# Kernel optimization log

Hardware: AMD Instinct MI355X
Metric: run time of the kernel (lower is better)

The kernel has to match this reference:

```python
import jax, jax.numpy as jnp
import numpy as np

D_MODEL = 1024
N_HEADS = 16
HEAD_DIM = D_MODEL // N_HEADS
D_FF = 4096
B, S = 2, 2048
EPS = 1e-6
NEG = -1e9


def setup_inputs() -> dict:
    key = jax.random.key(0)
    ks = jax.random.split(key, 16)
    sd = 1.0 / np.sqrt(D_MODEL)
    sf = 1.0 / np.sqrt(D_FF)
    inp = {
        "x": jax.random.normal(ks[0], (B, S, D_MODEL), jnp.float32),
        # causal mask, broadcastable over batch and heads
        "mask": jnp.tril(jnp.ones((S, S), jnp.bool_))[None, None, :, :],
        # attention projections, torch Linear layout [out, in]
        "Wq": jax.random.normal(ks[1], (D_MODEL, D_MODEL), jnp.float32) * sd,
        "bq": jnp.zeros((D_MODEL,), jnp.float32),
        "Wk": jax.random.normal(ks[2], (D_MODEL, D_MODEL), jnp.float32) * sd,
        "bk": jnp.zeros((D_MODEL,), jnp.float32),
        "Wv": jax.random.normal(ks[3], (D_MODEL, D_MODEL), jnp.float32) * sd,
        "bv": jnp.zeros((D_MODEL,), jnp.float32),
        "Wo": jax.random.normal(ks[4], (D_MODEL, D_MODEL), jnp.float32) * sd,
        "bo": jnp.zeros((D_MODEL,), jnp.float32),
        # layer norms
        "ln1_g": jnp.ones((D_MODEL,), jnp.float32),
        "ln1_b": jnp.zeros((D_MODEL,), jnp.float32),
        "ln2_g": jnp.ones((D_MODEL,), jnp.float32),
        "ln2_b": jnp.zeros((D_MODEL,), jnp.float32),
        # FFN
        "W1": jax.random.normal(ks[5], (D_FF, D_MODEL), jnp.float32) * sd,
        "b1": jnp.zeros((D_FF,), jnp.float32),
        "W2": jax.random.normal(ks[6], (D_MODEL, D_FF), jnp.float32) * sf,
        "b2": jnp.zeros((D_MODEL,), jnp.float32),
    }
    return inp


def _layer_norm(x, g, b):
    mu = jnp.mean(x, axis=-1, keepdims=True)
    var = jnp.var(x, axis=-1, keepdims=True)
    return (x - mu) * jax.lax.rsqrt(var + EPS) * g + b


def _linear(x, W, b):
    return jnp.einsum('...i,oi->...o', x, W) + b


def _attention(x, mask, Wq, bq, Wk, bk, Wv, bv, Wo, bo):
    Bsz, Sq, _ = x.shape
    q = _linear(x, Wq, bq).reshape(Bsz, Sq, N_HEADS, HEAD_DIM)
    k = _linear(x, Wk, bk).reshape(Bsz, Sq, N_HEADS, HEAD_DIM)
    v = _linear(x, Wv, bv).reshape(Bsz, Sq, N_HEADS, HEAD_DIM)
    # [B,H,S,S]
    scores = jnp.einsum('bqhd,bkhd->bhqk', q, k) / np.sqrt(HEAD_DIM)
    scores = jnp.where(mask, scores, NEG)
    weights = jax.nn.softmax(scores, axis=-1)
    ctx = jnp.einsum('bhqk,bkhd->bqhd', weights, v).reshape(Bsz, Sq, D_MODEL)
    return _linear(ctx, Wo, bo)


def reference(x, mask, Wq, bq, Wk, bk, Wv, bv, Wo, bo,
              ln1_g, ln1_b, ln2_g, ln2_b, W1, b1, W2, b2):
    # pre-LN attention block (dropout = identity at inference)
    h = _layer_norm(x, ln1_g, ln1_b)
    x = x + _attention(h, mask, Wq, bq, Wk, bk, Wv, bv, Wo, bo)
    # pre-LN FFN block
    h = _layer_norm(x, ln2_g, ln2_b)
    h = jax.nn.gelu(_linear(h, W1, b1), approximate=False)
    x = x + _linear(h, W2, b2)
    return x
```

## Files before the change

kernel.cpp:

```cpp
#include <hip/hip_runtime.h>
#include <hip/hip_bf16.h>
#include <cstdint>
#include <cstddef>

typedef unsigned short u16;
typedef __bf16 bf16x8 __attribute__((ext_vector_type(8)));
typedef float f32x4 __attribute__((ext_vector_type(4)));

#define D_MODEL 1024
#define D_FF    4096
#define BATCH   2
#define SEQ     2048
#define NH      16
#define HD      64
#define ROWS    (BATCH*SEQ)
#define QKVS    3072

__device__ __forceinline__ u16 f2bf(float f) {
    union { float f; uint32_t u; } v; v.f = f;
    uint32_t u = v.u;
    u += 0x7FFF + ((u >> 16) & 1);
    return (u16)(u >> 16);
}

__device__ __forceinline__ float bf2f(u16 u) {
    union { uint32_t u; float f; } v; v.u = (uint32_t)u << 16;
    return v.f;
}

__device__ __forceinline__ uint32_t cvtpk_bf16(float lo, float hi) {
    uint32_t r;
    asm("v_cvt_pk_bf16_f32 %0, %1, %2" : "=v"(r) : "v"(lo), "v"(hi));
    return r;
}

__device__ __forceinline__ bf16x8 ldg8(const u16* p) {
    return *reinterpret_cast<const bf16x8*>(p);
}

__device__ __forceinline__ f32x4 mfma16(bf16x8 a, bf16x8 b, f32x4 c) {
    return __builtin_amdgcn_mfma_f32_16x16x32_bf16(a, b, c, 0, 0, 0);
}

__device__ __forceinline__ void gld_lds16(const void* g, void* l) {
    __builtin_amdgcn_global_load_lds(
        (const __attribute__((address_space(1))) void*)g,
        (__attribute__((address_space(3))) void*)l, 16, 0, 0);
}

__device__ __forceinline__ float gelu_f(float x) {
    float u = fmaf(0.044715f * x, x * x, x);
    float z = fminf(-2.3022036f * u, 126.0f);
    float e = __builtin_amdgcn_exp2f(z);
    return x / (1.0f + e);
}

struct alignas(8) U16x4 { u16 x, y, z, w; };

__global__ __launch_bounds__(256) void prep(
    const float* __restrict__ s0, const float* __restrict__ s1,
    const float* __restrict__ s2, const float* __restrict__ s3,
    const float* __restrict__ s4, const float* __restrict__ s5,
    u16* __restrict__ wout,
    const float* __restrict__ x, const float* __restrict__ g1,
    const float* __restrict__ be1, u16* __restrict__ hbuf,
    const float* __restrict__ bq, const float* __restrict__ bk,
    const float* __restrict__ bv, float* __restrict__ bqkv)
{
    const size_t MM1 = 1 << 20;
    const int bid = blockIdx.x;
    const int t = threadIdx.x;

    if (bid < 12288) {
        size_t i = (size_t)bid * 1024 + t * 4;
        const float* src; size_t off;
        if      (i <     MM1) { src = s0; off = i; }
        else if (i < 2 * MM1) { src = s1; off = i - MM1; }
        else if (i < 3 * MM1) { src = s2; off = i - 2 * MM1; }
        else if (i < 4 * MM1) { src = s3; off = i - 3 * MM1; }
        else if (i < 8 * MM1) { src = s4; off = i - 4 * MM1; }
        else                  { src = s5; off = i - 8 * MM1; }
        float4 f = *reinterpret_cast<const float4*>(src + off);
        U16x4 o{ f2bf(f.x), f2bf(f.y), f2bf(f.z), f2bf(f.w) };
        *reinterpret_cast<U16x4*>(wout + i) = o;
    } else if (bid < 12288 + ROWS) {
        int row = bid - 12288;
        const float* xr = x + (size_t)row * D_MODEL;
        float4 v = *reinterpret_cast<const float4*>(xr + t * 4);
        float s = v.x + v.y + v.z + v.w;
        float q = v.x*v.x + v.y*v.y + v.z*v.z + v.w*v.w;
        #pragma unroll
        for (int off = 1; off < 64; off <<= 1) {
            s += __shfl_xor(s, off);
            q += __shfl_xor(q, off);
        }
        __shared__ float red[8];
        if ((t & 63) == 0) { red[(t >> 6) * 2] = s; red[(t >> 6) * 2 + 1] = q; }
        __syncthreads();
        float sum = red[0] + red[2] + red[4] + red[6];
        float sq  = red[1] + red[3] + red[5] + red[7];
        float mu  = sum * (1.0f / D_MODEL);
        float var = sq * (1.0f / D_MODEL) - mu * mu;
        float rstd = rsqrtf(var + 1e-6f);
        float4 gg = *reinterpret_cast<const float4*>(g1 + t * 4);
        float4 bb = *reinterpret_cast<const float4*>(be1 + t * 4);
        U16x4 o{ f2bf((v.x - mu) * rstd * gg.x + bb.x),
                 f2bf((v.y - mu) * rstd * gg.y + bb.y),
                 f2bf((v.z - mu) * rstd * gg.z + bb.z),
                 f2bf((v.w - mu) * rstd * gg.w + bb.w) };
        *reinterpret_cast<U16x4*>(hbuf + (size_t)row * D_MODEL + t * 4) = o;
    } else {
        int j = bid - (12288 + ROWS);
        const float* src = (j == 0) ? bq : (j == 1) ? bk : bv;
        float4 f = *reinterpret_cast<const float4*>(src + t * 4);
        *reinterpret_cast<float4*>(bqkv + j * 1024 + t * 4) = f;
    }
}

__global__ __launch_bounds__(256) void ln2_bf16(
    const u16* __restrict__ x, const float* __restrict__ g,
    const float* __restrict__ b, u16* __restrict__ out)
{
    int row = blockIdx.x;
    const u16* xr = x + (size_t)row * D_MODEL;
    int t = threadIdx.x;
    U16x4 u = *reinterpret_cast<const U16x4*>(xr + t * 4);
    float vx = bf2f(u.x), vy = bf2f(u.y), vz = bf2f(u.z), vw = bf2f(u.w);
    float s = vx + vy + vz + vw;
    float q = vx*vx + vy*vy + vz*vz + vw*vw;
    #pragma unroll
    for (int off = 1; off < 64; off <<= 1) {
        s += __shfl_xor(s, off);
        q += __shfl_xor(q, off);
    }
    __shared__ float red[8];
    if ((t & 63) == 0) { red[(t >> 6) * 2] = s; red[(t >> 6) * 2 + 1] = q; }
    __syncthreads();
    float sum = red[0] + red[2] + red[4] + red[6];
    float sq  = red[1] + red[3] + red[5] + red[7];
    float mu  = sum * (1.0f / D_MODEL);
    float var = sq * (1.0f / D_MODEL) - mu * mu;
    float rstd = rsqrtf(var + 1e-6f);
    float4 gg = *reinterpret_cast<const float4*>(g + t * 4);
    float4 bb = *reinterpret_cast<const float4*>(b + t * 4);
    U16x4 o{ f2bf((vx - mu) * rstd * gg.x + bb.x),
             f2bf((vy - mu) * rstd * gg.y + bb.y),
             f2bf((vz - mu) * rstd * gg.z + bb.z),
             f2bf((vw - mu) * rstd * gg.w + bb.w) };
    *reinterpret_cast<U16x4*>(out + (size_t)row * D_MODEL + t * 4) = o;
}

#define EPI_BF16   0
#define EPI_RESF32 1
#define EPI_GELU   2
#define EPI_PART   3
#define EPI_QKV    4
#define EPI_RESB16 5

template<int EPI>
__global__ __launch_bounds__(256, 4) void gemm97(
    const u16* __restrict__ A, const u16* __restrict__ B,
    const float* __restrict__ bias, const float* __restrict__ res,
    u16* __restrict__ outb, float* __restrict__ outf,
    int M, int N, int K, int KS)
{
    __shared__ u16 As[128 * 64];
    __shared__ u16 Bs[128 * 64];
    const int t = threadIdx.x;
    const int lane = t & 63, w = t >> 6;
    const int lr = lane & 15, lg = lane >> 4;
    const int wrr = (w >> 1) * 64, wcc = (w & 1) * 64;
    const int brow = blockIdx.x * 128, bcol = blockIdx.y * 128;
    const u16* Ag = A + (size_t)brow * KS;
    const u16* Bg = B + (size_t)bcol * KS;

    f32x4 acc[4][4] = {};
    const int NT = K >> 6;

    for (int kt = 0; kt < NT; ++kt) {
        #pragma unroll
        for (int c = 0; c < 4; ++c) {
            int f = c * 256 + t;
            int row = f >> 3, slot = f & 7;
            int sg = slot ^ (row & 7);
            gld_lds16(Ag + (size_t)row * KS + kt * 64 + sg * 8, As + f * 8);
            gld_lds16(Bg + (size_t)row * KS + kt * 64 + sg * 8, Bs + f * 8);
        }
        __syncthreads();

        bf16x8 af[4][2];
        #pragma unroll
        for (int mi = 0; mi < 4; ++mi) {
            int row = wrr + mi * 16 + lr;
            const u16* bp = As + row * 64;
            int key = row & 7;
            af[mi][0] = ldg8(bp + ((0 + lg) ^ key) * 8);
            af[mi][1] = ldg8(bp + ((4 + lg) ^ key) * 8);
        }
        __builtin_amdgcn_s_setprio(1);
        #pragma unroll
        for (int ni = 0; ni < 4; ++ni) {
            int row = wcc + ni * 16 + lr;
            const u16* bp = Bs + row * 64;
            int key = row & 7;
            bf16x8 b0 = ldg8(bp + ((0 + lg) ^ key) * 8);
            bf16x8 b1 = ldg8(bp + ((4 + lg) ^ key) * 8);
            #pragma unroll
            for (int mi = 0; mi < 4; ++mi) {
                acc[mi][ni] = mfma16(af[mi][0], b0, acc[mi][ni]);
                acc[mi][ni] = mfma16(af[mi][1], b1, acc[mi][ni]);
            }
        }
        __builtin_amdgcn_s_setprio(0);
        __syncthreads();
    }

    #pragma unroll
    for (int mi = 0; mi < 4; ++mi) {
        int r0 = brow + wrr + mi * 16 + lg * 4;
        #pragma unroll
        for (int ni = 0; ni < 4; ++ni) {
            int c = bcol + wcc + ni * 16 + lr;
            float bv = bias[c];
            if constexpr (EPI == EPI_QKV) {
                if (bcol >= 2048) {
                    U16x4 pk{ f2bf(acc[mi][ni][0] + bv), f2bf(acc[mi][ni][1] + bv),
                              f2bf(acc[mi][ni][2] + bv), f2bf(acc[mi][ni][3] + bv) };
                    int d = c - 2048;
                    int bb = r0 >> 11, s = r0 & 2047;
                    u16* vt = (u16*)outf;
                    *reinterpret_cast<U16x4*>(
                        vt + ((size_t)(bb * NH + (d >> 6)) * HD + (d & 63)) * SEQ + s) = pk;
                    continue;
                }
            }
            #pragma unroll
            for (int j = 0; j < 4; ++j) {
                float v = acc[mi][ni][j] + bv;
                size_t idx = (size_t)(r0 + j) * N + c;
                if constexpr (EPI == EPI_GELU) {
                    outb[idx] = f2bf(gelu_f(v));
                } else if constexpr (EPI == EPI_RESF32) {
                    outf[idx] = v + res[idx];
                } else {
                    outb[idx] = f2bf(v);
                }
            }
        }
    }
}

template<int EPI, int RM>
__global__ __launch_bounds__(256, 2) void gemm_bt(
    const u16* __restrict__ A, const u16* __restrict__ B,
    const float* __restrict__ bias, const float* __restrict__ res,
    u16* __restrict__ outb, float* __restrict__ outf,
    int M, int N, int K, int KS)
{
    __shared__ u16 As[2][128 * 64];
    __shared__ u16 Bs[2][128 * 64];
    const int t = threadIdx.x;
    const int lane = t & 63;
    const int w = t >> 6;
    const int lr = lane & 15, lg = lane >> 4;
    const int wrr = (w >> 1) * 64, wcc = (w & 1) * 64;
    const int brow = (RM ? blockIdx.x : blockIdx.y) * 128;
    const int bcol = (RM ? blockIdx.y : blockIdx.x) * 128;
    const int kz = blockIdx.z;
    const u16* Ag = A + (size_t)brow * KS + (size_t)kz * K;
    const u16* Bg = B + (size_t)bcol * KS + (size_t)kz * K;

    f32x4 acc[4][4] = {};

    const int NT = K >> 6;

    auto stage = [&](int buf, int kt) {
        const u16* ga = Ag + kt * 64;
        const u16* gb = Bg + kt * 64;
        u16* la = As[buf];
        u16* lb = Bs[buf];
        #pragma unroll
        for (int c = 0; c < 4; ++c) {
            int f = c * 256 + t;
            int row = f >> 3, slot = f & 7;
            int sg = slot ^ (row & 7);
            gld_lds16(ga + (size_t)row * KS + sg * 8, la + f * 8);
            gld_lds16(gb + (size_t)row * KS + sg * 8, lb + f * 8);
        }
    };

    auto compute = [&](int buf) {
        const u16* la = As[buf];
        const u16* lb = Bs[buf];
        bf16x8 af[4][2];
        #pragma unroll
        for (int mi = 0; mi < 4; ++mi) {
            int row = wrr + mi * 16 + lr;
            int base = row * 64;
            af[mi][0] = *reinterpret_cast<const bf16x8*>(la + base + ((0 + lg) ^ (row & 7)) * 8);
            af[mi][1] = *reinterpret_cast<const bf16x8*>(la + base + ((4 + lg) ^ (row & 7)) * 8);
        }
        __builtin_amdgcn_s_setprio(1);
        #pragma unroll
        for (int ni = 0; ni < 4; ++ni) {
            int row = wcc + ni * 16 + lr;
            int base = row * 64;
            bf16x8 b0 = *reinterpret_cast<const bf16x8*>(lb + base + ((0 + lg) ^ (row & 7)) * 8);
            bf16x8 b1 = *reinterpret_cast<const bf16x8*>(lb + base + ((4 + lg) ^ (row & 7)) * 8);
            #pragma unroll
            for (int mi = 0; mi < 4; ++mi) {
                acc[mi][ni] = mfma16(af[mi][0], b0, acc[mi][ni]);
                acc[mi][ni] = mfma16(af[mi][1], b1, acc[mi][ni]);
            }
        }
        __builtin_amdgcn_s_setprio(0);
    };

    stage(0, 0);
    if (NT > 1) {
        stage(1, 1);
        asm volatile("s_waitcnt vmcnt(8)" ::: "memory");
    } else {
        asm volatile("s_waitcnt vmcnt(0)" ::: "memory");
    }
    __builtin_amdgcn_s_barrier();

    for (int kt = 0; kt < NT; ++kt) {
        compute(kt & 1);
        if (kt + 1 == NT) break;
        __builtin_amdgcn_s_barrier();
        if (kt + 2 < NT) {
            stage(kt & 1, kt + 2);
            asm volatile("s_waitcnt vmcnt(8)" ::: "memory");
        } else {
            asm volatile("s_waitcnt vmcnt(0)" ::: "memory");
        }
        __builtin_amdgcn_s_barrier();
    }

    #pragma unroll
    for (int mi = 0; mi < 4; ++mi) {
        int r0 = brow + wrr + mi * 16 + lg * 4;
        #pragma unroll
        for (int ni = 0; ni < 4; ++ni) {
            int c = bcol + wcc + ni * 16 + lr;
            float bv = 0.f;
            if constexpr (EPI != EPI_PART) bv = bias[c];
            #pragma unroll
            for (int j = 0; j < 4; ++j) {
                float v = acc[mi][ni][j] + bv;
                size_t idx = (size_t)(r0 + j) * N + c;
                if constexpr (EPI == EPI_GELU) {
                    outb[idx] = f2bf(gelu_f(v));
                } else if constexpr (EPI == EPI_RESF32) {
                    outf[idx] = v + res[idx];
                } else if constexpr (EPI == EPI_RESB16) {
                    outb[idx] = f2bf(v + res[idx]);
                } else if constexpr (EPI == EPI_PART) {
                    outb[idx + (size_t)kz * M * N] = f2bf(v);
                } else {
                    outb[idx] = f2bf(v);
                }
            }
        }
    }
}

__global__ void ffn2_reduce(const u16* __restrict__ p,
                            const float* __restrict__ b2,
                            const u16* __restrict__ x2,
                            float* __restrict__ out)
{
    size_t i = ((size_t)blockIdx.x * 256 + threadIdx.x) * 4;
    U16x4 a0 = *reinterpret_cast<const U16x4*>(p + i);
    U16x4 a1 = *reinterpret_cast<const U16x4*>(p + (size_t)ROWS * D_MODEL + i);
    U16x4 rr = *reinterpret_cast<const U16x4*>(x2 + i);
    float4 bb = *reinterpret_cast<const float4*>(b2 + (i & (D_MODEL - 1)));
    float4 o;
    o.x = bf2f(a0.x) + bf2f(a1.x) + bf2f(rr.x) + bb.x;
    o.y = bf2f(a0.y) + bf2f(a1.y) + bf2f(rr.y) + bb.y;
    o.z = bf2f(a0.z) + bf2f(a1.z) + bf2f(rr.z) + bb.z;
    o.w = bf2f(a0.w) + bf2f(a1.w) + bf2f(rr.w) + bb.w;
    *reinterpret_cast<float4*>(out + i) = o;
}

#define QBLK  64
#define KVBLK 64

__global__ __launch_bounds__(256, 3) void attn8(
    const u16* __restrict__ QKV, const u16* __restrict__ VT,
    u16* __restrict__ O)
{
    __shared__ u16 Ks[3][64 * 64];
    __shared__ u16 Vs[2][64 * 64];
    __shared__ u16 Pl[4][16 * 72];

    const int i  = blockIdx.x;
    const int bh = blockIdx.y;
    const int b = bh >> 4, h = bh & 15;
    const int qta = 31 - i;
    const int qtb = i;
    const int q0a = qta * QBLK, q0b = qtb * QBLK;
    const int t = threadIdx.x;
    const int lane = t & 63, w = t >> 6;
    const int lr = lane & 15, lg = lane >> 4;

    const size_t rowbase = (size_t)b * SEQ;
    const u16* Qg = QKV + rowbase * QKVS + h * HD;
    const u16* Kg = Qg + 1024;
    const u16* Vg = VT + (size_t)bh * HD * SEQ;

    const u16* qpa = Qg + (size_t)(q0a + w * 16 + lr) * QKVS;
    const u16* qpb = Qg + (size_t)(q0b + w * 16 + lr) * QKVS;
    bf16x8 qa0 = ldg8(qpa + lg * 8), qa1 = ldg8(qpa + 32 + lg * 8);
    bf16x8 qb0 = ldg8(qpb + lg * 8), qb1 = ldg8(qpb + 32 + lg * 8);

    f32x4 oa[4] = {}, ob[4] = {};
    float lsa[4] = {}, lsb[4] = {};

    const int ntiles = qta + 1;
    u16* Pw = Pl[w];
    const float SC = 0.125f * 1.44269504089f;

    auto stageK = [&](int buf, int tt) {
        const int kv0 = tt * KVBLK;
        #pragma unroll
        for (int c = 0; c < 2; ++c) {
            int f = c * 256 + t;
            int row = f >> 3, slot = f & 7;
            int sgk = slot ^ ((row >> 2) & 7);
            gld_lds16(Kg + (size_t)(kv0 + row) * QKVS + sgk * 8, Ks[buf] + f * 8);
        }
    };
    auto stageV = [&](int buf, int tt) {
        const int kv0 = tt * KVBLK;
        #pragma unroll
        for (int c = 0; c < 2; ++c) {
            int f = c * 256 + t;
            int row = f >> 3, slot = f & 7;
            int sgv = slot ^ (row & 7);
            gld_lds16(Vg + (size_t)row * SEQ + kv0 + sgv * 8, Vs[buf] + f * 8);
        }
    };

    auto qtile = [&](bf16x8 qf0, bf16x8 qf1, f32x4* o, float* ls,
                     int q0, int kv0, bool diag, const u16* kb, const u16* vb) {
        f32x4 s[4] = {};
        __builtin_amdgcn_s_setprio(1);
        #pragma unroll
        for (int ni = 0; ni < 4; ++ni) {
            int row = lr * 4 + ni;
            const u16* base = kb + row * 64;
            int key = (row >> 2) & 7;
            bf16x8 k0 = *reinterpret_cast<const bf16x8*>(base + ((0 + lg) ^ key) * 8);
            bf16x8 k1 = *reinterpret_cast<const bf16x8*>(base + ((4 + lg) ^ key) * 8);
            s[ni] = mfma16(qf0, k0, s[ni]);
            s[ni] = mfma16(qf1, k1, s[ni]);
        }
        __builtin_amdgcn_s_setprio(0);

        #pragma unroll
        for (int j = 0; j < 4; ++j) {
            int qi = q0 + w * 16 + lg * 4 + j;
            float p0 = __builtin_amdgcn_exp2f(s[0][j] * SC);
            float p1 = __builtin_amdgcn_exp2f(s[1][j] * SC);
            float p2 = __builtin_amdgcn_exp2f(s[2][j] * SC);
            float p3 = __builtin_amdgcn_exp2f(s[3][j] * SC);
            if (diag) {
                int kvb = kv0 + lr * 4;
                p0 = (kvb     <= qi) ? p0 : 0.f;
                p1 = (kvb + 1 <= qi) ? p1 : 0.f;
                p2 = (kvb + 2 <= qi) ? p2 : 0.f;
                p3 = (kvb + 3 <= qi) ? p3 : 0.f;
            }
            ls[j] += (p0 + p1) + (p2 + p3);
            uint2 pk = make_uint2(cvtpk_bf16(p0, p1), cvtpk_bf16(p2, p3));
            *reinterpret_cast<uint2*>(&Pw[(lg * 4 + j) * 72 + lr * 4]) = pk;
        }

        bf16x8 pa0 = *reinterpret_cast<const bf16x8*>(Pw + lr * 72 + lg * 8);
        bf16x8 pa1 = *reinterpret_cast<const bf16x8*>(Pw + lr * 72 + 32 + lg * 8);
        __builtin_amdgcn_s_setprio(1);
        #pragma unroll
        for (int ni = 0; ni < 4; ++ni) {
            int row = ni * 16 + lr;
            const u16* base = vb + row * 64;
            bf16x8 v0 = *reinterpret_cast<const bf16x8*>(base + ((0 + lg) ^ (row & 7)) * 8);
            bf16x8 v1 = *reinterpret_cast<const bf16x8*>(base + ((4 + lg) ^ (row & 7)) * 8);
            o[ni] = mfma16(pa0, v0, o[ni]);
            o[ni] = mfma16(pa1, v1, o[ni]);
        }
        __builtin_amdgcn_s_setprio(0);
    };

    stageV(0, 0);
    stageK(0, 0);
    stageK(1, 1);

    for (int tt = 0; tt < ntiles; ++tt) {
        __builtin_amdgcn_s_barrier();
        if (tt + 1 < ntiles) stageV((tt + 1) & 1, tt + 1);
        if (tt + 2 < ntiles) stageK((tt + 2) % 3, tt + 2);
        if (tt + 2 < ntiles)
            asm volatile("s_waitcnt vmcnt(6)" ::: "memory");
        else if (tt + 1 < ntiles)
            asm volatile("s_waitcnt vmcnt(4)" ::: "memory");
        else
            asm volatile("s_waitcnt vmcnt(0)" ::: "memory");

        const int kv0 = tt * KVBLK;
        const u16* kb = Ks[tt % 3];
        const u16* vb = Vs[tt & 1];

        qtile(qa0, qa1, oa, lsa, q0a, kv0, tt == qta, kb, vb);
        if (tt <= qtb)
            qtile(qb0, qb1, ob, lsb, q0b, kv0, tt == qtb, kb, vb);
    }

    #pragma unroll
    for (int j = 0; j < 4; ++j) {
        float va = lsa[j], vb2 = lsb[j];
        va += __shfl_xor(va, 1); vb2 += __shfl_xor(vb2, 1);
        va += __shfl_xor(va, 2); vb2 += __shfl_xor(vb2, 2);
        va += __shfl_xor(va, 4); vb2 += __shfl_xor(vb2, 4);
        va += __shfl_xor(va, 8); vb2 += __shfl_xor(vb2, 8);
        lsa[j] = va; lsb[j] = vb2;
    }

    u16* Oa = O + (rowbase + q0a + w * 16) * D_MODEL + h * HD;
    u16* Ob = O + (rowbase + q0b + w * 16) * D_MODEL + h * HD;
    #pragma unroll
    for (int j = 0; j < 4; ++j) {
        float inva = 1.0f / lsa[j];
        float invb = 1.0f / lsb[j];
        int r = (lg * 4 + j) * D_MODEL;
        #pragma unroll
        for (int ni = 0; ni < 4; ++ni) {
            Oa[r + ni * 16 + lr] = f2bf(oa[ni][j] * inva);
            Ob[r + ni * 16 + lr] = f2bf(ob[ni][j] * invb);
        }
    }
}

extern "C" void kernel_launch(void* const* d_in, const int* in_sizes, int n_in,
                              void* d_out, int out_size, void* d_ws, size_t ws_size,
                              hipStream_t stream)
{
    (void)in_sizes; (void)n_in; (void)out_size; (void)ws_size;
    const float* x   = (const float*)d_in[0];
    const float* Wq  = (const float*)d_in[2];
    const float* bq  = (const float*)d_in[3];
    const float* Wk  = (const float*)d_in[4];
    const float* bk  = (const float*)d_in[5];
    const float* Wv  = (const float*)d_in[6];
    const float* bv  = (const float*)d_in[7];
    const float* Wo  = (const float*)d_in[8];
    const float* bo  = (const float*)d_in[9];
    const float* g1  = (const float*)d_in[10];
    const float* be1 = (const float*)d_in[11];
    const float* g2  = (const float*)d_in[12];
    const float* be2 = (const float*)d_in[13];
    const float* W1  = (const float*)d_in[14];
    const float* b1  = (const float*)d_in[15];
    const float* W2  = (const float*)d_in[16];
    const float* b2  = (const float*)d_in[17];
    float* out = (float*)d_out;

    const size_t MM = 1 << 20;
    u16* Wqkv_b = (u16*)d_ws;
    u16* Wo_b = Wqkv_b + 3 * MM;
    u16* W1_b = Wo_b + MM;
    u16* W2_b = W1_b + 4 * MM;
    u16* hbuf = W2_b + 4 * MM;
    u16* QKVb = hbuf + 4 * MM;
    u16* ctx  = QKVb + 12 * MM;
    u16* ffn1 = ctx + 4 * MM;
    u16* x2   = ffn1 + 16 * MM;
    float* bqkv = (float*)(x2 + 4 * MM);
    u16* VTb  = (u16*)(bqkv + 4096);
    u16* fpart = QKVb;

    prep<<<12288 + ROWS + 3, 256, 0, stream>>>(Wq, Wk, Wv, Wo, W1, W2, Wqkv_b,
                                               x, g1, be1, hbuf, bq, bk, bv, bqkv);

    dim3 gqkv(ROWS / 128, QKVS / 128);
    gemm97<EPI_QKV><<<gqkv, 256, 0, stream>>>(hbuf, Wqkv_b, bqkv, nullptr,
                                              QKVb, (float*)VTb, ROWS, QKVS, 1024, 1024);

    dim3 ga(SEQ / QBLK / 2, BATCH * NH);
    attn8<<<ga, 256, 0, stream>>>(QKVb, VTb, ctx);

    dim3 gq(ROWS / 128, D_MODEL / 128);
    gemm_bt<EPI_RESB16, 1><<<gq, 256, 0, stream>>>(ctx, Wo_b, bo, x, x2, nullptr,
                                                   ROWS, D_MODEL, 1024, 1024);

    ln2_bf16<<<ROWS, 256, 0, stream>>>(x2, g2, be2, hbuf);

    dim3 gf1(ROWS / 128, D_FF / 128);
    gemm97<EPI_GELU><<<gf1, 256, 0, stream>>>(hbuf, W1_b, b1, nullptr, ffn1, nullptr,
                                              ROWS, D_FF, 1024, 1024);

    dim3 gf2(D_MODEL / 128, ROWS / 128, 2);
    gemm_bt<EPI_PART, 0><<<gf2, 256, 0, stream>>>(ffn1, W2_b, nullptr, nullptr,
                                                  fpart, nullptr, ROWS, D_MODEL, 2048, 4096);
    ffn2_reduce<<<(ROWS * D_MODEL) / 1024, 256, 0, stream>>>(fpart, b2, x2, out);
}
```

Baseline: 215.6 us.

## Split attention KV tiles across two blocks and merge partial results

Each attention block pair now handles only every other KV tile (selected by blockIdx.z), which doubles the grid to raise occupancy across the GPU's compute units. Unnormalized partial outputs go to a scratch buffer as bf16, and the row sums go to a separate float buffer. A new merge kernel then adds the two partials and normalizes them into ctx. This adds an extra launch, extra global traffic and bf16 rounding of the unnormalized partials. It relies on the softmax using a fixed scale rather than a running max, so the partials can simply be added.

```diff
diff --git a/kernel.cpp b/kernel.cpp
--- a/kernel.cpp
+++ b/kernel.cpp
@@ -387,9 +387,9 @@
 #define QBLK  64
 #define KVBLK 64
 
-__global__ __launch_bounds__(256, 3) void attn8(
+__global__ __launch_bounds__(256, 3) void attn10(
     const u16* __restrict__ QKV, const u16* __restrict__ VT,
-    u16* __restrict__ O)
+    u16* __restrict__ pO, float* __restrict__ pL)
 {
     __shared__ u16 Ks[3][64 * 64];
     __shared__ u16 Vs[2][64 * 64];
@@ -397,6 +397,7 @@
 
     const int i  = blockIdx.x;
     const int bh = blockIdx.y;
+    const int z  = blockIdx.z;
     const int b = bh >> 4, h = bh & 15;
     const int qta = 31 - i;
     const int qtb = i;
@@ -418,7 +419,7 @@
     f32x4 oa[4] = {}, ob[4] = {};
     float lsa[4] = {}, lsb[4] = {};
 
-    const int ntiles = qta + 1;
+    const int nk = (qta - z) / 2 + 1;
     u16* Pw = Pl[w];
     const float SC = 0.125f * 1.44269504089f;
 
@@ -493,24 +494,25 @@
         __builtin_amdgcn_s_setprio(0);
     };
 
-    stageV(0, 0);
-    stageK(0, 0);
-    stageK(1, 1);
-
-    for (int tt = 0; tt < ntiles; ++tt) {
+    stageV(0, z);
+    stageK(0, z);
+    if (nk > 1) stageK(1, z + 2);
+
+    for (int k = 0; k < nk; ++k) {
+        const int tt = z + 2 * k;
         __builtin_amdgcn_s_barrier();
-        if (tt + 1 < ntiles) stageV((tt + 1) & 1, tt + 1);
-        if (tt + 2 < ntiles) stageK((tt + 2) % 3, tt + 2);
-        if (tt + 2 < ntiles)
+        if (k + 1 < nk) stageV((k + 1) & 1, tt + 2);
+        if (k + 2 < nk) stageK((k + 2) % 3, tt + 4);
+        if (k + 2 < nk)
             asm volatile("s_waitcnt vmcnt(6)" ::: "memory");
-        else if (tt + 1 < ntiles)
+        else if (k + 1 < nk)
             asm volatile("s_waitcnt vmcnt(4)" ::: "memory");
         else
             asm volatile("s_waitcnt vmcnt(0)" ::: "memory");
 
         const int kv0 = tt * KVBLK;
-        const u16* kb = Ks[tt % 3];
-        const u16* vb = Vs[tt & 1];
+        const u16* kb = Ks[k % 3];
+        const u16* vb = Vs[k & 1];
 
         qtile(qa0, qa1, oa, lsa, q0a, kv0, tt == qta, kb, vb);
         if (tt <= qtb)
@@ -527,19 +529,44 @@
         lsa[j] = va; lsb[j] = vb2;
     }
 
-    u16* Oa = O + (rowbase + q0a + w * 16) * D_MODEL + h * HD;
-    u16* Ob = O + (rowbase + q0b + w * 16) * D_MODEL + h * HD;
+    u16* Oa = pO + (size_t)z * ROWS * D_MODEL + (rowbase + q0a + w * 16) * D_MODEL + h * HD;
+    u16* Ob = pO + (size_t)z * ROWS * D_MODEL + (rowbase + q0b + w * 16) * D_MODEL + h * HD;
+    float* La = pL + (size_t)z * ROWS * NH + (rowbase + q0a + w * 16) * NH + h;
+    float* Lb = pL + (size_t)z * ROWS * NH + (rowbase + q0b + w * 16) * NH + h;
     #pragma unroll
     for (int j = 0; j < 4; ++j) {
-        float inva = 1.0f / lsa[j];
-        float invb = 1.0f / lsb[j];
         int r = (lg * 4 + j) * D_MODEL;
         #pragma unroll
         for (int ni = 0; ni < 4; ++ni) {
-            Oa[r + ni * 16 + lr] = f2bf(oa[ni][j] * inva);
-            Ob[r + ni * 16 + lr] = f2bf(ob[ni][j] * invb);
-        }
-    }
+            Oa[r + ni * 16 + lr] = f2bf(oa[ni][j]);
+            Ob[r + ni * 16 + lr] = f2bf(ob[ni][j]);
+        }
+        if (lr == 0) {
+            La[(lg * 4 + j) * NH] = lsa[j];
+            Lb[(lg * 4 + j) * NH] = lsb[j];
+        }
+    }
+}
+
+__global__ __launch_bounds__(256) void attn_merge(
+    const u16* __restrict__ pO, const float* __restrict__ pL,
+    u16* __restrict__ ctx)
+{
+    const int row = blockIdx.x;
+    const int t = threadIdx.x;
+    const int c = t * 4;
+    const int h = c >> 6;
+    float l0 = pL[(size_t)row * NH + h];
+    float l1 = pL[(size_t)ROWS * NH + (size_t)row * NH + h];
+    float inv = 1.0f / (l0 + l1);
+    size_t idx = (size_t)row * D_MODEL + c;
+    U16x4 a0 = *reinterpret_cast<const U16x4*>(pO + idx);
+    U16x4 a1 = *reinterpret_cast<const U16x4*>(pO + (size_t)ROWS * D_MODEL + idx);
+    U16x4 o{ f2bf((bf2f(a0.x) + bf2f(a1.x)) * inv),
+             f2bf((bf2f(a0.y) + bf2f(a1.y)) * inv),
+             f2bf((bf2f(a0.z) + bf2f(a1.z)) * inv),
+             f2bf((bf2f(a0.w) + bf2f(a1.w)) * inv) };
+    *reinterpret_cast<U16x4*>(ctx + idx) = o;
 }
 
 extern "C" void kernel_launch(void* const* d_in, const int* in_sizes, int n_in,
@@ -578,6 +605,8 @@
     u16* x2   = ffn1 + 16 * MM;
     float* bqkv = (float*)(x2 + 4 * MM);
     u16* VTb  = (u16*)(bqkv + 4096);
+    float* pL = (float*)(VTb + 4 * MM);
+    u16* pO   = ffn1;
     u16* fpart = QKVb;
 
     prep<<<12288 + ROWS + 3, 256, 0, stream>>>(Wq, Wk, Wv, Wo, W1, W2, Wqkv_b,
@@ -587,8 +616,9 @@
     gemm97<EPI_QKV><<<gqkv, 256, 0, stream>>>(hbuf, Wqkv_b, bqkv, nullptr,
                                               QKVb, (float*)VTb, ROWS, QKVS, 1024, 1024);
 
-    dim3 ga(SEQ / QBLK / 2, BATCH * NH);
-    attn8<<<ga, 256, 0, stream>>>(QKVb, VTb, ctx);
+    dim3 ga(SEQ / QBLK / 2, BATCH * NH, 2);
+    attn10<<<ga, 256, 0, stream>>>(QKVb, VTb, pO, pL);
+    attn_merge<<<ROWS, 256, 0, stream>>>(pO, pL, ctx);
 
     dim3 gq(ROWS / 128, D_MODEL / 128);
     gemm_bt<EPI_RESB16, 1><<<gq, 256, 0, stream>>>(ctx, Wo_b, bo, x, x2, nullptr,
```

After: 226.9 us. 5.3% more time.
